# Optimization experiments

Hardware: AMD Instinct MI355X
Metric: run time of the kernel (lower is better)

## Reference

```python
import jax, jax.numpy as jnp
import numpy as np

N = 20000      # nodes
E = 320000     # edges
IN = 300       # input_channel
HID = 100      # hidden_channel (= heads*out_channels with heads=1)
R = 50         # num_relations
B = 8          # num_bases (the 4th positional arg 'heads'=8 lands on num_bases in PyG RGATConv)
HEADS = 1
CLS = 3
Q = 64         # number of query (aspect) nodes
EPS = 1e-16


def setup_inputs() -> dict:
    key = jax.random.key(0)
    ks = jax.random.split(key, 16)
    x = jax.random.normal(ks[0], (N, IN), jnp.float32)
    edge_index = jax.random.randint(ks[1], (2, E), 0, N)
    edge_type = jax.random.randint(ks[2], (E,), 0, R)
    query_indices = jax.random.randint(ks[3], (Q,), 0, N)

    def w(k, shape, scale):
        return jax.random.normal(k, shape, jnp.float32) * scale

    comp1 = w(ks[4], (R, B), 0.3)
    basis1 = w(ks[5], (B, IN, HEADS * HID), 1.0 / np.sqrt(IN))
    q1 = w(ks[6], (HEADS * HID, HEADS), 0.1)
    k1 = w(ks[7], (HEADS * HID, HEADS), 0.1)
    b1 = jnp.zeros((HEADS * HID,), jnp.float32)
    comp2 = w(ks[8], (R, B), 0.3)
    basis2 = w(ks[9], (B, HID, HEADS * HID), 1.0 / np.sqrt(HID))
    q2 = w(ks[10], (HEADS * HID, HEADS), 0.1)
    k2 = w(ks[11], (HEADS * HID, HEADS), 0.1)
    b2 = jnp.zeros((HEADS * HID,), jnp.float32)
    Wl = w(ks[12], (CLS, HID), 1.0 / np.sqrt(HID))
    bl = jnp.zeros((CLS,), jnp.float32)
    return dict(x=x, edge_index=edge_index, edge_type=edge_type,
                query_indices=query_indices,
                comp1=comp1, basis1=basis1, q1=q1, k1=k1, b1=b1,
                comp2=comp2, basis2=basis2, q2=q2, k2=k2, b2=b2,
                Wl=Wl, bl=bl)


def segment_softmax(alpha, seg, num_segments):
    # numerically-stable softmax over edges grouped by destination node
    m = jax.ops.segment_max(alpha, seg, num_segments=num_segments)  # [N, H]
    e = jnp.exp(alpha - m[seg])
    s = jax.ops.segment_sum(e, seg, num_segments=num_segments)
    return e / (s[seg] + EPS)


def rgat_conv(x, edge_index, edge_type, comp, basis, q, k, b):
    # basis-decomposed per-relation weight: [R, in, H*out]
    W = jnp.einsum('rb,bio->rio', comp, basis)
    # transform every node under every relation once, then gather per edge
    xt = jnp.einsum('ni,rio->nro', x, W)          # [N, R, H*out]
    src, dst = edge_index[0], edge_index[1]        # j -> i (source_to_target)
    xi = xt[dst, edge_type]                        # [E, H*out]
    xj = xt[src, edge_type]                        # [E, H*out]
    qi = xi @ q                                    # [E, H]
    kj = xj @ k                                    # [E, H]
    alpha = jax.nn.leaky_relu(qi + kj, 0.2)        # additive self-attention
    alpha = segment_softmax(alpha, dst, N)         # across-relation softmax
    msg = xj.reshape(E, HEADS, HID) * alpha[:, :, None]
    out = jax.ops.segment_sum(msg, dst, num_segments=N)  # [N, H, out]
    return out.reshape(N, HEADS * HID) + b         # concat=True


def reference(x, edge_index, edge_type, query_indices,
              comp1, basis1, q1, k1, b1,
              comp2, basis2, q2, k2, b2, Wl, bl):
    h = jax.nn.relu(rgat_conv(x, edge_index, edge_type, comp1, basis1, q1, k1, b1))
    h = jax.nn.relu(rgat_conv(h, edge_index, edge_type, comp2, basis2, q2, k2, b2))
    pooled = h[query_indices].mean(axis=0)          # [HID]
    return pooled @ Wl.T + bl                       # [CLS]
```

## Files before the change

kernel.cpp:

```cpp
#include <hip/hip_runtime.h>
#include <math.h>

#define N_NODES 20000
#define E_EDGES 320000
#define IN_CH   300
#define HID     100
#define R_REL   50
#define NB      8
#define CLS     3
#define NQ      64
#define OUTW    800
#define ZW      128
#define SCAN_BLKS ((N_NODES + 255) / 256)

typedef unsigned short ushort_t;
typedef __attribute__((ext_vector_type(8))) short     short8;
typedef __attribute__((ext_vector_type(8))) unsigned short ushort8;
typedef __attribute__((ext_vector_type(4))) float     f32x4;
typedef __attribute__((ext_vector_type(2))) float     f32x2;

__device__ __forceinline__ ushort_t f2bf_rne(float f) {
    unsigned u = __float_as_uint(f);
    unsigned r = (u + 0x7fffu + ((u >> 16) & 1u)) >> 16;
    return (ushort_t)r;
}
__device__ __forceinline__ float bf2f(ushort_t u) {
    return __uint_as_float((unsigned)u << 16);
}

__global__ __launch_bounds__(256) void zero_deg2(int* __restrict__ dd,
                                                 int* __restrict__ ds) {
    int i = blockIdx.x * 256 + threadIdx.x;
    if (i < N_NODES) { dd[i] = 0; ds[i] = 0; }
}

__global__ __launch_bounds__(256) void hist2_kernel(
        const int* __restrict__ ei, int* __restrict__ dd,
        int* __restrict__ ds) {
    int e = blockIdx.x * 256 + threadIdx.x;
    if (e < E_EDGES) {
        atomicAdd(&dd[ei[E_EDGES + e]], 1);
        atomicAdd(&ds[ei[e]], 1);
    }
}

__global__ __launch_bounds__(256) void scan1_kernel(
        const int* __restrict__ deg, int* __restrict__ rowptr,
        int* __restrict__ bsum) {
    __shared__ int s[256];
    int tid = threadIdx.x;
    int idx = blockIdx.x * 256 + tid;
    int v = (idx < N_NODES) ? deg[idx] : 0;
    s[tid] = v; __syncthreads();
    #pragma unroll
    for (int off = 1; off < 256; off <<= 1) {
        int t = (tid >= off) ? s[tid - off] : 0;
        __syncthreads();
        s[tid] += t;
        __syncthreads();
    }
    if (idx < N_NODES) rowptr[idx] = s[tid] - v;
    if (tid == 255) bsum[blockIdx.x] = s[255];
}

__global__ __launch_bounds__(128) void scan2_kernel(int* __restrict__ bsum,
                                                    int* __restrict__ rowptr) {
    __shared__ int s[128];
    int tid = threadIdx.x;
    int v = (tid < SCAN_BLKS) ? bsum[tid] : 0;
    s[tid] = v; __syncthreads();
    #pragma unroll
    for (int off = 1; off < 128; off <<= 1) {
        int t = (tid >= off) ? s[tid - off] : 0;
        __syncthreads();
        s[tid] += t;
        __syncthreads();
    }
    if (tid < SCAN_BLKS) bsum[tid] = s[tid] - v;
    if (tid == 0) rowptr[N_NODES] = E_EDGES;
}

__global__ __launch_bounds__(256) void scan3_kernel(
        int* __restrict__ rowptr, const int* __restrict__ bsum,
        int* __restrict__ cursor) {
    int idx = blockIdx.x * 256 + threadIdx.x;
    if (idx < N_NODES) {
        int v = rowptr[idx] + bsum[blockIdx.x];
        rowptr[idx] = v;
        cursor[idx] = v;
    }
}

__global__ __launch_bounds__(256) void scatter_both(
        const int* __restrict__ ei, const int* __restrict__ et,
        int* __restrict__ cur_d, int* __restrict__ cur_s,
        int* __restrict__ skey, int* __restrict__ skey_s) {
    int e = blockIdx.x * 256 + threadIdx.x;
    if (e >= E_EDGES) return;
    int s = ei[e], d = ei[E_EDGES + e], rt = et[e];
    int p = atomicAdd(&cur_d[d], 1);
    skey[p] = (s << 6) | rt;
    int qp = atomicAdd(&cur_s[s], 1);
    skey_s[qp] = (p << 6) | rt;
}

__global__ __launch_bounds__(256) void split_bt_kernel(
        const float* __restrict__ basis, ushort_t* __restrict__ Bt,
        int K, int Kp) {
    int idx = blockIdx.x * 256 + threadIdx.x;
    if (idx >= OUTW * Kp) return;
    int n = idx / Kp, k = idx - n * Kp;
    int b = n / HID, o = n - b * HID;
    float v = 0.f;
    if (k < K) v = basis[((size_t)b * K + k) * HID + o];
    Bt[idx] = f2bf_rne(v);
}

#define BM 64
#define BN 160
#define NCB (OUTW / BN)
__global__ __launch_bounds__(256) void gemm_mfma(
        const float* __restrict__ A, const ushort_t* __restrict__ Bt,
        ushort_t* __restrict__ xbh, int M, int K, int Kp, int do_relu) {
    __shared__ ushort_t As[64 * 328];
    __shared__ ushort_t Bs[BN][32];
    int tid  = threadIdx.x;
    int lane = tid & 63, wave = tid >> 6;
    int ml = lane & 15, quad = lane >> 4;
    int wr = (wave >> 1) * 32, wc = (wave & 1) * 80;
    int row0 = blockIdx.x * BM;
    int SW = Kp + 8;
    int ksteps = Kp >> 5;

    {
        int ra = tid >> 2;
        int gr = row0 + ra;
        const float* ar = A + (size_t)gr * K;
        for (int c = (tid & 3); c * 8 < Kp; c += 4) {
            int kb = c * 8;
            float vals[8];
            if (gr < M) {
                if (kb + 8 <= K) {
                    float4 f0 = *(const float4*)&ar[kb];
                    float4 f1 = *(const float4*)&ar[kb + 4];
                    vals[0]=f0.x; vals[1]=f0.y; vals[2]=f0.z; vals[3]=f0.w;
                    vals[4]=f1.x; vals[5]=f1.y; vals[6]=f1.z; vals[7]=f1.w;
                } else {
                    #pragma unroll
                    for (int i = 0; i < 8; i++)
                        vals[i] = (kb + i < K) ? ar[kb + i] : 0.f;
                }
                if (do_relu)
                    #pragma unroll
                    for (int i = 0; i < 8; i++) vals[i] = fmaxf(vals[i], 0.f);
            } else {
                #pragma unroll
                for (int i = 0; i < 8; i++) vals[i] = 0.f;
            }
            ushort8 hv;
            #pragma unroll
            for (int i = 0; i < 8; i++) hv[i] = f2bf_rne(vals[i]);
            *(ushort8*)&As[ra * SW + kb] = hv;
        }
    }

    int pq = quad ^ (ml & 3);
    for (int cb = 0; cb < NCB; cb++) {
        int col0 = cb * BN;
        f32x4 acc[2][5] = {};
        for (int ks = 0; ks < ksteps; ks++) {
            int k0 = ks << 5;
            __syncthreads();
            for (int t = tid; t < 640; t += 256) {
                int rb = t >> 2, ch = t & 3;
                int ph = ch ^ (rb & 3);
                ushort8 vh = *(const ushort8*)&Bt[(size_t)(col0 + rb) * Kp + k0 + ch * 8];
                *(ushort8*)&Bs[rb][ph * 8] = vh;
            }
            __syncthreads();
            short8 af[2], bf[5];
            #pragma unroll
            for (int mt = 0; mt < 2; mt++)
                af[mt] = *(const short8*)&As[(wr + mt * 16 + ml) * SW + k0 + quad * 8];
            #pragma unroll
            for (int nt = 0; nt < 5; nt++)
                bf[nt] = *(const short8*)&Bs[wc + nt * 16 + ml][pq * 8];
            #pragma unroll
            for (int mt = 0; mt < 2; mt++)
                #pragma unroll
                for (int nt = 0; nt < 5; nt++)
                    acc[mt][nt] = __builtin_amdgcn_mfma_f32_16x16x32_bf16(af[mt], bf[nt], acc[mt][nt], 0, 0, 0);
        }
        #pragma unroll
        for (int mt = 0; mt < 2; mt++) {
            #pragma unroll
            for (int nt = 0; nt < 5; nt++) {
                #pragma unroll
                for (int r = 0; r < 4; r++) {
                    int grow = row0 + wr + mt * 16 + quad * 4 + r;
                    if (grow < M)
                        xbh[(size_t)grow * OUTW + col0 + wc + nt * 16 + ml] =
                            f2bf_rne(acc[mt][nt][r]);
                }
            }
        }
    }
}

__global__ __launch_bounds__(256) void qbkb_kernel(
        const float* __restrict__ basis, const float* __restrict__ q,
        const float* __restrict__ k, float* __restrict__ qb,
        float* __restrict__ kb, int K) {
    int idx = blockIdx.x * 256 + threadIdx.x;
    if (idx >= K * NB) return;
    int kk = idx >> 3, b = idx & 7;
    const float* br = basis + ((size_t)b * K + kk) * HID;
    float aq = 0.f, ak = 0.f;
    for (int o = 0; o < HID; o++) {
        float v = br[o];
        aq = fmaf(v, q[o], aq);
        ak = fmaf(v, k[o], ak);
    }
    qb[idx] = aq; kb[idx] = ak;
}

__global__ __launch_bounds__(256) void qk2_kernel(
        const float* __restrict__ x, const float* __restrict__ qb,
        const float* __restrict__ kb, float* __restrict__ xbq,
        float* __restrict__ xbk, int K, int do_relu) {
    __shared__ float sqb[320 * NB], skb[320 * NB];
    int tid = threadIdx.x;
    for (int i = tid; i < K * NB; i += 256) { sqb[i] = qb[i]; skb[i] = kb[i]; }
    __syncthreads();
    int idx = blockIdx.x * 256 + tid;
    if (idx >= N_NODES * NB) return;
    int n = idx >> 3, b = idx & 7;
    const float* xr = x + (size_t)n * K;
    float aq = 0.f, ak = 0.f;
    for (int kk = 0; kk < K; kk++) {
        float v = xr[kk];
        if (do_relu) v = fmaxf(v, 0.f);
        aq = fmaf(v, sqb[kk * NB + b], aq);
        ak = fmaf(v, skb[kk * NB + b], ak);
    }
    xbq[idx] = aq;
    xbk[idx] = ak;
}

__global__ __launch_bounds__(256) void compute_z(
        const int* __restrict__ rowptr_s, const int* __restrict__ skey_s,
        const float* __restrict__ comp, const ushort_t* __restrict__ xbh,
        ushort_t* __restrict__ Z) {
    int wave = threadIdx.x >> 6, lane = threadIdx.x & 63;
    int s = blockIdx.x * 4 + wave;
    if (s >= N_NODES) return;
    int beg = rowptr_s[s], end = rowptr_s[s + 1];
    if (beg == end) return;
    int o = lane * 2;
    f32x2 xrow[NB];
    if (lane < 50) {
        #pragma unroll
        for (int b = 0; b < NB; b++) {
            ushort2 xx = *(const ushort2*)&xbh[(size_t)s * OUTW + b * HID + o];
            xrow[b].x = bf2f(xx.x);
            xrow[b].y = bf2f(xx.y);
        }
    }
    for (int p = beg; p < end; p++) {
        int key = skey_s[p];
        int zpos = key >> 6, rt = key & 63;
        const float* cr = comp + rt * NB;
        if (lane < 50) {
            f32x2 z = {0.f, 0.f};
            #pragma unroll
            for (int b = 0; b < NB; b++) z += cr[b] * xrow[b];
            ushort2 zz;
            zz.x = f2bf_rne(z.x);
            zz.y = f2bf_rne(z.y);
            *(ushort2*)&Z[(size_t)zpos * ZW + o] = zz;
        }
    }
}

__global__ __launch_bounds__(256) void msg_soft(
        const int* __restrict__ rowptr, const int* __restrict__ skey,
        const float* __restrict__ comp, const ushort_t* __restrict__ Z,
        const float* __restrict__ xbq, const float* __restrict__ xbk,
        const float* __restrict__ bias, float* __restrict__ h) {
    int wave = threadIdx.x >> 6, lane = threadIdx.x & 63;
    int d = blockIdx.x * 4 + wave;
    if (d >= N_NODES) return;
    int beg = rowptr[d], end = rowptr[d + 1];

    float4 qd0 = *(const float4*)&xbq[d * NB];
    float4 qd1 = *(const float4*)&xbq[d * NB + 4];

    f32x2 acc = {0.f, 0.f};
    float m = -1e30f, l = 0.f;
    int o = lane * 2;

    for (int c0 = beg; c0 < end; c0 += 64) {
        int p = c0 + lane;
        bool valid = p < end;
        float a = -1e30f;
        if (valid) {
            int key = skey[p];
            int s = key >> 6, rt = key & 63;
            const float4 c0v = *(const float4*)&comp[rt * NB];
            const float4 c1v = *(const float4*)&comp[rt * NB + 4];
            const float4 k0v = *(const float4*)&xbk[s * NB];
            const float4 k1v = *(const float4*)&xbk[s * NB + 4];
            float qi = c0v.x*qd0.x + c0v.y*qd0.y + c0v.z*qd0.z + c0v.w*qd0.w
                     + c1v.x*qd1.x + c1v.y*qd1.y + c1v.z*qd1.z + c1v.w*qd1.w;
            float kj = c0v.x*k0v.x + c0v.y*k0v.y + c0v.z*k0v.z + c0v.w*k0v.w
                     + c1v.x*k1v.x + c1v.y*k1v.y + c1v.z*k1v.z + c1v.w*k1v.w;
            a = qi + kj;
            a = a > 0.f ? a : 0.2f * a;
        }
        float cm = a;
        #pragma unroll
        for (int off = 32; off; off >>= 1) cm = fmaxf(cm, __shfl_xor(cm, off));
        float M = fmaxf(m, cm);
        float scale = __expf(m - M);
        acc *= scale; l *= scale; m = M;
        float wgt = valid ? __expf(a - M) : 0.f;
        float cs = wgt;
        #pragma unroll
        for (int off = 32; off; off >>= 1) cs += __shfl_xor(cs, off);
        l += cs;
        int cnt = end - c0; if (cnt > 64) cnt = 64;
        for (int j = 0; j < cnt; j++) {
            float wj = __shfl(wgt, j);
            if (lane < 50) {
                ushort2 zz = *(const ushort2*)&Z[(size_t)(c0 + j) * ZW + o];
                f32x2 zv = {bf2f(zz.x), bf2f(zz.y)};
                acc += wj * zv;
            }
        }
    }
    if (lane < 50) {
        float inv = 1.f / (l + 1e-16f);
        f32x2 r;
        r.x = bias[o]     + acc.x * inv;
        r.y = bias[o + 1] + acc.y * inv;
        *(f32x2*)&h[(size_t)d * HID + o] = r;
    }
}

__global__ __launch_bounds__(128) void head_kernel(
        const float* __restrict__ h2, const int* __restrict__ qidx,
        const float* __restrict__ Wl, const float* __restrict__ bl,
        float* __restrict__ out) {
    __shared__ float pooled[HID];
    int tid = threadIdx.x;
    if (tid < HID) {
        float s = 0.f;
        for (int i = 0; i < NQ; i++)
            s += fmaxf(h2[(size_t)qidx[i] * HID + tid], 0.f);
        pooled[tid] = s * (1.0f / NQ);
    }
    __syncthreads();
    if (tid < CLS) {
        float s = bl[tid];
        for (int o = 0; o < HID; o++) s = fmaf(pooled[o], Wl[tid * HID + o], s);
        out[tid] = s;
    }
}

extern "C" void kernel_launch(void* const* d_in, const int* in_sizes, int n_in,
                              void* d_out, int out_size, void* d_ws, size_t ws_size,
                              hipStream_t stream) {
    const float* x      = (const float*)d_in[0];
    const int*   ei     = (const int*)  d_in[1];
    const int*   et     = (const int*)  d_in[2];
    const int*   qidx   = (const int*)  d_in[3];
    const float* comp1  = (const float*)d_in[4];
    const float* basis1 = (const float*)d_in[5];
    const float* q1     = (const float*)d_in[6];
    const float* k1     = (const float*)d_in[7];
    const float* b1     = (const float*)d_in[8];
    const float* comp2  = (const float*)d_in[9];
    const float* basis2 = (const float*)d_in[10];
    const float* q2     = (const float*)d_in[11];
    const float* k2     = (const float*)d_in[12];
    const float* b2     = (const float*)d_in[13];
    const float* Wl     = (const float*)d_in[14];
    const float* bl     = (const float*)d_in[15];
    float* out = (float*)d_out;

    const int KP1 = 320, KP2 = 128;

    char* w = (char*)d_ws;
    size_t off = 0;
    auto alloc = [&](size_t nbytes) {
        void* p = (void*)(w + off);
        off += ((nbytes + 255) / 256) * 256;
        return p;
    };
    ushort_t* xbh    = (ushort_t*)alloc((size_t)N_NODES * OUTW * 2);
    ushort_t* Z      = (ushort_t*)alloc((size_t)E_EDGES * ZW * 2);
    float*    h1     = (float*)alloc((size_t)N_NODES * HID * 4);
    float*    h2     = (float*)alloc((size_t)N_NODES * HID * 4);
    ushort_t* Bt     = (ushort_t*)alloc((size_t)OUTW * KP1 * 2);
    float*    xbq    = (float*)alloc((size_t)N_NODES * NB * 4);
    float*    xbk    = (float*)alloc((size_t)N_NODES * NB * 4);
    float*    qb     = (float*)alloc((size_t)KP1 * NB * 4);
    float*    kb     = (float*)alloc((size_t)KP1 * NB * 4);
    int*      deg_d  = (int*)alloc(N_NODES * 4);
    int*      deg_s  = (int*)alloc(N_NODES * 4);
    int*      rp_d   = (int*)alloc((N_NODES + 1) * 4);
    int*      rp_s   = (int*)alloc((N_NODES + 1) * 4);
    int*      cur_d  = (int*)alloc(N_NODES * 4);
    int*      cur_s  = (int*)alloc(N_NODES * 4);
    int*      bsum   = (int*)alloc(SCAN_BLKS * 4);
    int*      skey   = (int*)alloc(E_EDGES * 4);
    int*      skey_s = (int*)alloc(E_EDGES * 4);

    zero_deg2<<<SCAN_BLKS, 256, 0, stream>>>(deg_d, deg_s);
    hist2_kernel<<<(E_EDGES + 255) / 256, 256, 0, stream>>>(ei, deg_d, deg_s);
    scan1_kernel<<<SCAN_BLKS, 256, 0, stream>>>(deg_d, rp_d, bsum);
    scan2_kernel<<<1, 128, 0, stream>>>(bsum, rp_d);
    scan3_kernel<<<SCAN_BLKS, 256, 0, stream>>>(rp_d, bsum, cur_d);
    scan1_kernel<<<SCAN_BLKS, 256, 0, stream>>>(deg_s, rp_s, bsum);
    scan2_kernel<<<1, 128, 0, stream>>>(bsum, rp_s);
    scan3_kernel<<<SCAN_BLKS, 256, 0, stream>>>(rp_s, bsum, cur_s);
    scatter_both<<<(E_EDGES + 255) / 256, 256, 0, stream>>>(ei, et, cur_d, cur_s, skey, skey_s);

    auto layer = [&](const float* input, int K, int Kp, int relu_in,
                     const float* comp, const float* basis, const float* q,
                     const float* k, const float* bias, float* hout) {
        int nb = OUTW * Kp;
        split_bt_kernel<<<(nb + 255) / 256, 256, 0, stream>>>(basis, Bt, K, Kp);
        gemm_mfma<<<(N_NODES + BM - 1) / BM, 256, 0, stream>>>(input, Bt, xbh, N_NODES, K, Kp, relu_in);
        qbkb_kernel<<<(K * NB + 255) / 256, 256, 0, stream>>>(basis, q, k, qb, kb, K);
        qk2_kernel<<<(N_NODES * NB + 255) / 256, 256, 0, stream>>>(input, qb, kb, xbq, xbk, K, relu_in);
        compute_z<<<(N_NODES + 3) / 4, 256, 0, stream>>>(rp_s, skey_s, comp, xbh, Z);
        msg_soft<<<(N_NODES + 3) / 4, 256, 0, stream>>>(rp_d, skey, comp, Z, xbq, xbk, bias, hout);
    };

    layer(x,  IN_CH, KP1, 0, comp1, basis1, q1, k1, b1, h1);
    layer(h1, HID,   KP2, 1, comp2, basis2, q2, k2, b2, h2);
    head_kernel<<<1, 128, 0, stream>>>(h2, qidx, Wl, bl, out);
}
```

Baseline: 444.7 us.

## Batch CSR scans for both edge sets and shrink GEMM tile using direct-to-LDS loads

The dst and src prefix scans are merged into single launches that cover both sets, cutting six scan launches to three and using separate block-sum buffers. The GEMM row tile is halved from 64 to 32, doubling the block count for better occupancy across CUs. B tiles are now copied straight into LDS with global_load_lds instead of going through registers, which drops the XOR swizzle and may add LDS bank conflicts. Each B tile is also reused across fewer rows, so more B traffic goes to global memory.

```diff
diff --git a/kernel.cpp b/kernel.cpp
--- a/kernel.cpp
+++ b/kernel.cpp
@@ -44,12 +44,16 @@
     }
 }
 
-__global__ __launch_bounds__(256) void scan1_kernel(
-        const int* __restrict__ deg, int* __restrict__ rowptr,
-        int* __restrict__ bsum) {
+__global__ __launch_bounds__(256) void scan1_both(
+        const int* __restrict__ deg_d, int* __restrict__ rp_d, int* __restrict__ bsum_d,
+        const int* __restrict__ deg_s, int* __restrict__ rp_s, int* __restrict__ bsum_s) {
+    int set = blockIdx.x / SCAN_BLKS, blk = blockIdx.x % SCAN_BLKS;
+    const int* deg = set ? deg_s : deg_d;
+    int* rowptr    = set ? rp_s  : rp_d;
+    int* bsum      = set ? bsum_s : bsum_d;
     __shared__ int s[256];
     int tid = threadIdx.x;
-    int idx = blockIdx.x * 256 + tid;
+    int idx = blk * 256 + tid;
     int v = (idx < N_NODES) ? deg[idx] : 0;
     s[tid] = v; __syncthreads();
     #pragma unroll
@@ -60,11 +64,14 @@
         __syncthreads();
     }
     if (idx < N_NODES) rowptr[idx] = s[tid] - v;
-    if (tid == 255) bsum[blockIdx.x] = s[255];
-}
-
-__global__ __launch_bounds__(128) void scan2_kernel(int* __restrict__ bsum,
-                                                    int* __restrict__ rowptr) {
+    if (tid == 255) bsum[blk] = s[255];
+}
+
+__global__ __launch_bounds__(128) void scan2_both(
+        int* __restrict__ bsum_d, int* __restrict__ rp_d,
+        int* __restrict__ bsum_s, int* __restrict__ rp_s) {
+    int* bsum   = blockIdx.x ? bsum_s : bsum_d;
+    int* rowptr = blockIdx.x ? rp_s   : rp_d;
     __shared__ int s[128];
     int tid = threadIdx.x;
     int v = (tid < SCAN_BLKS) ? bsum[tid] : 0;
@@ -80,12 +87,16 @@
     if (tid == 0) rowptr[N_NODES] = E_EDGES;
 }
 
-__global__ __launch_bounds__(256) void scan3_kernel(
-        int* __restrict__ rowptr, const int* __restrict__ bsum,
-        int* __restrict__ cursor) {
-    int idx = blockIdx.x * 256 + threadIdx.x;
+__global__ __launch_bounds__(256) void scan3_both(
+        int* __restrict__ rp_d, const int* __restrict__ bsum_d, int* __restrict__ cur_d,
+        int* __restrict__ rp_s, const int* __restrict__ bsum_s, int* __restrict__ cur_s) {
+    int set = blockIdx.x / SCAN_BLKS, blk = blockIdx.x % SCAN_BLKS;
+    int* rowptr      = set ? rp_s   : rp_d;
+    const int* bsum  = set ? bsum_s : bsum_d;
+    int* cursor      = set ? cur_s  : cur_d;
+    int idx = blk * 256 + threadIdx.x;
     if (idx < N_NODES) {
-        int v = rowptr[idx] + bsum[blockIdx.x];
+        int v = rowptr[idx] + bsum[blk];
         rowptr[idx] = v;
         cursor[idx] = v;
     }
@@ -116,27 +127,27 @@
     Bt[idx] = f2bf_rne(v);
 }
 
-#define BM 64
+#define BM 32
 #define BN 160
 #define NCB (OUTW / BN)
 __global__ __launch_bounds__(256) void gemm_mfma(
         const float* __restrict__ A, const ushort_t* __restrict__ Bt,
         ushort_t* __restrict__ xbh, int M, int K, int Kp, int do_relu) {
-    __shared__ ushort_t As[64 * 328];
-    __shared__ ushort_t Bs[BN][32];
+    __shared__ ushort_t As[BM * 328];
+    __shared__ ushort_t Bs[BN * 32];
     int tid  = threadIdx.x;
     int lane = tid & 63, wave = tid >> 6;
     int ml = lane & 15, quad = lane >> 4;
-    int wr = (wave >> 1) * 32, wc = (wave & 1) * 80;
+    int wr = (wave >> 1) * 16, wc = (wave & 1) * 80;
     int row0 = blockIdx.x * BM;
     int SW = Kp + 8;
     int ksteps = Kp >> 5;
 
     {
-        int ra = tid >> 2;
+        int ra = tid >> 3;
         int gr = row0 + ra;
         const float* ar = A + (size_t)gr * K;
-        for (int c = (tid & 3); c * 8 < Kp; c += 4) {
+        for (int c = (tid & 7); c * 8 < Kp; c += 8) {
             int kb = c * 8;
             float vals[8];
             if (gr < M) {
@@ -164,44 +175,38 @@
         }
     }
 
-    int pq = quad ^ (ml & 3);
     for (int cb = 0; cb < NCB; cb++) {
         int col0 = cb * BN;
-        f32x4 acc[2][5] = {};
+        f32x4 acc[5] = {};
         for (int ks = 0; ks < ksteps; ks++) {
             int k0 = ks << 5;
             __syncthreads();
             for (int t = tid; t < 640; t += 256) {
                 int rb = t >> 2, ch = t & 3;
-                int ph = ch ^ (rb & 3);
-                ushort8 vh = *(const ushort8*)&Bt[(size_t)(col0 + rb) * Kp + k0 + ch * 8];
-                *(ushort8*)&Bs[rb][ph * 8] = vh;
+                __builtin_amdgcn_global_load_lds(
+                    (const __attribute__((address_space(1))) unsigned int*)
+                        &Bt[(size_t)(col0 + rb) * Kp + k0 + ch * 8],
+                    (__attribute__((address_space(3))) unsigned int*)&Bs[t * 8],
+                    16, 0, 0);
             }
             __syncthreads();
-            short8 af[2], bf[5];
-            #pragma unroll
-            for (int mt = 0; mt < 2; mt++)
-                af[mt] = *(const short8*)&As[(wr + mt * 16 + ml) * SW + k0 + quad * 8];
+            short8 af, bf[5];
+            af = *(const short8*)&As[(wr + ml) * SW + k0 + quad * 8];
             #pragma unroll
             for (int nt = 0; nt < 5; nt++)
-                bf[nt] = *(const short8*)&Bs[wc + nt * 16 + ml][pq * 8];
+                bf[nt] = *(const short8*)&Bs[(wc + nt * 16 + ml) * 32 + quad * 8];
             #pragma unroll
-            for (int mt = 0; mt < 2; mt++)
-                #pragma unroll
-                for (int nt = 0; nt < 5; nt++)
-                    acc[mt][nt] = __builtin_amdgcn_mfma_f32_16x16x32_bf16(af[mt], bf[nt], acc[mt][nt], 0, 0, 0);
+            for (int nt = 0; nt < 5; nt++)
+                acc[nt] = __builtin_amdgcn_mfma_f32_16x16x32_bf16(af, bf[nt], acc[nt], 0, 0, 0);
         }
         #pragma unroll
-        for (int mt = 0; mt < 2; mt++) {
+        for (int nt = 0; nt < 5; nt++) {
             #pragma unroll
-            for (int nt = 0; nt < 5; nt++) {
-                #pragma unroll
-                for (int r = 0; r < 4; r++) {
-                    int grow = row0 + wr + mt * 16 + quad * 4 + r;
-                    if (grow < M)
-                        xbh[(size_t)grow * OUTW + col0 + wc + nt * 16 + ml] =
-                            f2bf_rne(acc[mt][nt][r]);
-                }
+            for (int r = 0; r < 4; r++) {
+                int grow = row0 + wr + quad * 4 + r;
+                if (grow < M)
+                    xbh[(size_t)grow * OUTW + col0 + wc + nt * 16 + ml] =
+                        f2bf_rne(acc[nt][r]);
             }
         }
     }
@@ -412,18 +417,16 @@
     int*      rp_s   = (int*)alloc((N_NODES + 1) * 4);
     int*      cur_d  = (int*)alloc(N_NODES * 4);
     int*      cur_s  = (int*)alloc(N_NODES * 4);
-    int*      bsum   = (int*)alloc(SCAN_BLKS * 4);
+    int*      bsum_d = (int*)alloc(SCAN_BLKS * 4);
+    int*      bsum_s = (int*)alloc(SCAN_BLKS * 4);
     int*      skey   = (int*)alloc(E_EDGES * 4);
     int*      skey_s = (int*)alloc(E_EDGES * 4);
 
     zero_deg2<<<SCAN_BLKS, 256, 0, stream>>>(deg_d, deg_s);
     hist2_kernel<<<(E_EDGES + 255) / 256, 256, 0, stream>>>(ei, deg_d, deg_s);
-    scan1_kernel<<<SCAN_BLKS, 256, 0, stream>>>(deg_d, rp_d, bsum);
-    scan2_kernel<<<1, 128, 0, stream>>>(bsum, rp_d);
-    scan3_kernel<<<SCAN_BLKS, 256, 0, stream>>>(rp_d, bsum, cur_d);
-    scan1_kernel<<<SCAN_BLKS, 256, 0, stream>>>(deg_s, rp_s, bsum);
-    scan2_kernel<<<1, 128, 0, stream>>>(bsum, rp_s);
-    scan3_kernel<<<SCAN_BLKS, 256, 0, stream>>>(rp_s, bsum, cur_s);
+    scan1_both<<<2 * SCAN_BLKS, 256, 0, stream>>>(deg_d, rp_d, bsum_d, deg_s, rp_s, bsum_s);
+    scan2_both<<<2, 128, 0, stream>>>(bsum_d, rp_d, bsum_s, rp_s);
+    scan3_both<<<2 * SCAN_BLKS, 256, 0, stream>>>(rp_d, bsum_d, cur_d, rp_s, bsum_s, cur_s);
     scatter_both<<<(E_EDGES + 255) / 256, 256, 0, stream>>>(ei, et, cur_d, cur_s, skey, skey_s);
 
     auto layer = [&](const float* input, int K, int Kp, int relu_in,
```

Result: faster. 412.8 us (-7.2%).
